# Kernel tuning notes

Hardware: AMD Instinct MI355X
Metric: run time of the kernel (lower is better)

Reference implementation:

```python
import jax, jax.numpy as jnp
import numpy as np

PAD = float(-2**32 + 1)


def setup_inputs() -> dict:
    key = jax.random.key(0)
    ks = jax.random.split(key, 10)
    B, S, D = 8, 1024, 1024
    s = 0.02  # keep projections in sane range
    return {
        "Q": jax.random.normal(ks[0], (B, S, D), jnp.float32),
        "K": jax.random.normal(ks[1], (B, S, D), jnp.float32),
        "V": jax.random.normal(ks[2], (B, S, D), jnp.float32),
        "WQ": jax.random.normal(ks[3], (D, D), jnp.float32) * s,
        "bQ": jnp.zeros((D,), jnp.float32),
        "WK": jax.random.normal(ks[4], (D, D), jnp.float32) * s,
        "bK": jnp.zeros((D,), jnp.float32),
        "WV": jax.random.normal(ks[5], (D, D), jnp.float32) * s,
        "bV": jnp.zeros((D,), jnp.float32),
        "WO": jax.random.normal(ks[6], (D, D), jnp.float32) * s,
        "bO": jnp.zeros((D,), jnp.float32),
        "h": 16,
    }


def reference(Q, K, V, WQ, bQ, WK, bK, WV, bV, WO, bO, h):
    B, S, D = Q.shape
    dk = D // h
    # Dense projections with relu activation (as in the Keras layer)
    Qp = jax.nn.relu(Q @ WQ + bQ)
    Kp = jax.nn.relu(K @ WK + bK)
    Vp = jax.nn.relu(V @ WV + bV)
    # tf.concat(tf.split(x, h, axis=2), axis=0): head-major stacking -> (h, B, S, dk)
    qh = Qp.reshape(B, S, h, dk).transpose(2, 0, 1, 3)
    kh = Kp.reshape(B, S, h, dk).transpose(2, 0, 1, 3)
    vh = Vp.reshape(B, S, h, dk).transpose(2, 0, 1, 3)
    # scaled dot product; NOTE: source scales by 1/sqrt(d_model), not 1/sqrt(d_k)
    scores = jnp.einsum('hbqd,hbkd->hbqk', qh, kh) / jnp.sqrt(jnp.float32(D))
    # key padding mask: zero key rows -> large negative
    kmask = jnp.sum(jnp.abs(kh), axis=-1) != 0  # (h,B,Tk)
    scores = jnp.where(kmask[:, :, None, :], scores, PAD)
    w = jax.nn.softmax(scores, axis=-1)
    # query padding mask: zero query rows -> zero weights
    qmask = jnp.sign(jnp.sum(jnp.abs(qh), axis=-1))  # (h,B,Tq), 0/1
    w = w * qmask[:, :, :, None]
    # dropout_prob = 0.0 -> identity
    out = jnp.einsum('hbqk,hbkd->hbqd', w, vh)
    # tf.concat(tf.split(dot_product, h, axis=0), axis=2) -> (B,S,h*dk)
    out = out.transpose(1, 2, 0, 3).reshape(B, S, D)
    return jax.nn.relu(out @ WO + bO)
```

## Files before the change

### kernel.cpp

```cpp
#include <hip/hip_runtime.h>
#include <hip/hip_bf16.h>
#include <cstdint>

#define DEV __device__ __forceinline__

typedef __attribute__((ext_vector_type(4))) float f32x4;
typedef __attribute__((ext_vector_type(8))) short b16x8;
typedef __attribute__((ext_vector_type(4))) unsigned short u16x4;
typedef __attribute__((ext_vector_type(8))) unsigned short u16x8;
typedef __attribute__((ext_vector_type(2))) unsigned int u32x2;

typedef __attribute__((address_space(1))) void gvoid_t;
typedef __attribute__((address_space(3))) void lvoid_t;

static constexpr int Bsz = 8, Ssz = 1024, Dsz = 1024;
static constexpr int Mrows = Bsz * Ssz;

DEV void gld16(const void* g, void* l) {
  __builtin_amdgcn_global_load_lds((gvoid_t*)(uintptr_t)g,
                                   (lvoid_t*)(unsigned)(uintptr_t)l, 16, 0, 0);
}

DEV unsigned short f2bf(float x) {
  unsigned int u = __float_as_uint(x);
  u += 0x7fffu + ((u >> 16) & 1u);
  return (unsigned short)(u >> 16);
}

DEV unsigned int cvt2(float lo, float hi) {
  __hip_bfloat162 h = __float22bfloat162_rn(make_float2(lo, hi));
  unsigned int u;
  __builtin_memcpy(&u, &h, 4);
  return u;
}

__global__ __launch_bounds__(256) void wconv_kernel(
    const float* __restrict__ WQ, const float* __restrict__ WK,
    const float* __restrict__ WV, const float* __restrict__ WO,
    unsigned short* __restrict__ Wt) {
  __shared__ float tile[64][65];
  const int w = blockIdx.z;
  const float* W = (w == 0) ? WQ : (w == 1) ? WK : (w == 2) ? WV : WO;
  const int k0 = blockIdx.x * 64, n0 = blockIdx.y * 64;
  const int t = threadIdx.x;
  {
    const int r = t >> 4;
    const int c = (t & 15) * 4;
#pragma unroll
    for (int i = 0; i < 4; ++i) {
      f32x4 v = *(const f32x4*)(W + (size_t)(k0 + i * 16 + r) * Dsz + n0 + c);
      tile[i * 16 + r][c + 0] = v[0];
      tile[i * 16 + r][c + 1] = v[1];
      tile[i * 16 + r][c + 2] = v[2];
      tile[i * 16 + r][c + 3] = v[3];
    }
  }
  __syncthreads();
  {
    const int n = t >> 2;
    const int ks = (t & 3) * 16;
    unsigned short* dst =
        Wt + (size_t)w * Dsz * Dsz + (size_t)(n0 + n) * Dsz + k0 + ks;
#pragma unroll
    for (int j = 0; j < 16; j += 4) {
      u16x4 p;
#pragma unroll
      for (int jj = 0; jj < 4; ++jj) p[jj] = f2bf(tile[ks + j + jj][n]);
      *(u16x4*)(dst + j) = p;
    }
  }
}

template <bool A_FP32, int OUT_MODE>
DEV void gemm_body(unsigned short* __restrict__ Asl,
                   unsigned short* __restrict__ Bsl,
                   const void* __restrict__ A_,
                   const unsigned short* __restrict__ Bt,
                   const float* __restrict__ bias, void* __restrict__ C_,
                   int m0, int n0, float outscale) {
  constexpr int Kd = 1024, Nd = 1024;
  const int t = threadIdx.x, lane = t & 63, wave = t >> 6;
  const int grp = lane >> 4, r16 = lane & 15;
  const int wm = wave >> 1, wn = wave & 1;
  const int swz = (r16 & 7) << 4;
  f32x4 acc[4][4] = {};
  for (int kt = 0; kt < Kd; kt += 64) {
#pragma unroll
    for (int j = 0; j < 4; ++j) {
      int chunk = (wave * 4 + j) * 64 + lane;
      int row = chunk >> 3, c = chunk & 7;
      int csw = c ^ (row & 7);
      gld16(Bt + (size_t)(n0 + row) * Kd + kt + csw * 8,
            (char*)Bsl + (wave * 4 + j) * 1024);
      if constexpr (!A_FP32) {
        gld16((const unsigned short*)A_ + (size_t)(m0 + row) * Kd + kt + csw * 8,
              (char*)Asl + (wave * 4 + j) * 1024);
      }
    }
    if constexpr (A_FP32) {
      const float* A = (const float*)A_;
#pragma unroll
      for (int it = 0; it < 4; ++it) {
        int chunk = it * 256 + t;
        int row = chunk >> 3, c = chunk & 7;
        int csw = c ^ (row & 7);
        const float* src = A + (size_t)(m0 + row) * Kd + kt + csw * 8;
        f32x4 v0 = *(const f32x4*)src;
        f32x4 v1 = *(const f32x4*)(src + 4);
        u32x2 w0, w1;
        w0[0] = cvt2(v0[0], v0[1]);
        w0[1] = cvt2(v0[2], v0[3]);
        w1[0] = cvt2(v1[0], v1[1]);
        w1[1] = cvt2(v1[2], v1[3]);
        *(u32x2*)((char*)Asl + chunk * 16) = w0;
        *(u32x2*)((char*)Asl + chunk * 16 + 8) = w1;
      }
    }
    __syncthreads();
#pragma unroll
    for (int cs = 0; cs < 2; ++cs) {
      b16x8 af[4], bfr[4];
#pragma unroll
      for (int mi = 0; mi < 4; ++mi)
        af[mi] = *(const b16x8*)((char*)Asl + (wm * 64 + mi * 16 + r16) * 128 +
                                 ((cs * 64 + grp * 16) ^ swz));
#pragma unroll
      for (int ni = 0; ni < 4; ++ni)
        bfr[ni] = *(const b16x8*)((char*)Bsl + (wn * 64 + ni * 16 + r16) * 128 +
                                  ((cs * 64 + grp * 16) ^ swz));
#pragma unroll
      for (int mi = 0; mi < 4; ++mi)
#pragma unroll
        for (int ni = 0; ni < 4; ++ni)
          acc[mi][ni] = __builtin_amdgcn_mfma_f32_16x16x32_bf16(
              af[mi], bfr[ni], acc[mi][ni], 0, 0, 0);
    }
    __syncthreads();
  }
#pragma unroll
  for (int mi = 0; mi < 4; ++mi) {
#pragma unroll
    for (int ni = 0; ni < 4; ++ni) {
      int col = n0 + wn * 64 + ni * 16 + r16;
      float bv = bias[col];
      int row0 = m0 + wm * 64 + mi * 16 + grp * 4;
      if constexpr (OUT_MODE == 2) {
        int bb = row0 >> 10, s = row0 & 1023;
        u16x4 pk;
#pragma unroll
        for (int r = 0; r < 4; ++r)
          pk[r] = f2bf(fmaxf(acc[mi][ni][r] + bv, 0.0f) * outscale);
        *(u16x4*)((unsigned short*)C_ +
                  (((size_t)(bb * 1024 + col)) << 10) + s) = pk;
      } else {
#pragma unroll
        for (int r = 0; r < 4; ++r) {
          float v = fmaxf(acc[mi][ni][r] + bv, 0.0f) * outscale;
          if constexpr (OUT_MODE == 1)
            ((unsigned short*)C_)[(size_t)(row0 + r) * Nd + col] = f2bf(v);
          else
            ((float*)C_)[(size_t)(row0 + r) * Nd + col] = v;
        }
      }
    }
  }
}

static constexpr float QSCALE = 0.03125f * 1.4426950408889634f;

__global__ __launch_bounds__(256) void proj3_kernel(
    const float* __restrict__ Q, const float* __restrict__ K,
    const float* __restrict__ V, const unsigned short* __restrict__ Wt,
    const float* __restrict__ bQ, const float* __restrict__ bK,
    const float* __restrict__ bV, unsigned short* __restrict__ Qp,
    unsigned short* __restrict__ Kp, unsigned short* __restrict__ VpT) {
  __shared__ unsigned short Asl[128 * 64] __attribute__((aligned(16)));
  __shared__ unsigned short Bsl[128 * 64] __attribute__((aligned(16)));
  const size_t DD = (size_t)Dsz * Dsz;
  const int bid = blockIdx.x;
  const int id2 = (bid & 7) * 64 + (bid >> 3);
  const int n0 = (id2 & 7) * 128, m0 = (id2 >> 3) * 128;
  const int z = blockIdx.z;
  if (z == 0)
    gemm_body<true, 1>(Asl, Bsl, Q, Wt, bQ, Qp, m0, n0, QSCALE);
  else if (z == 1)
    gemm_body<true, 1>(Asl, Bsl, K, Wt + DD, bK, Kp, m0, n0, 1.0f);
  else
    gemm_body<true, 2>(Asl, Bsl, V, Wt + 2 * DD, bV, VpT, m0, n0, 1.0f);
}

__global__ __launch_bounds__(256) void out_gemm_kernel(
    const unsigned short* __restrict__ AO,
    const unsigned short* __restrict__ WOt, const float* __restrict__ bO,
    float* __restrict__ Out) {
  __shared__ unsigned short Asl[128 * 64] __attribute__((aligned(16)));
  __shared__ unsigned short Bsl[128 * 64] __attribute__((aligned(16)));
  const int bid = blockIdx.x;
  const int id2 = (bid & 7) * 64 + (bid >> 3);
  const int n0 = (id2 & 7) * 128, m0 = (id2 >> 3) * 128;
  gemm_body<false, 0>(Asl, Bsl, AO, WOt, bO, Out, m0, n0, 1.0f);
}

__global__ __launch_bounds__(512, 4) void attn_kernel(
    const unsigned short* __restrict__ Qp, const unsigned short* __restrict__ Kp,
    const unsigned short* __restrict__ VpT, unsigned short* __restrict__ AO) {
  __shared__ unsigned short Ks[2][64 * 64] __attribute__((aligned(16)));
  __shared__ unsigned short Vs[2][64 * 64] __attribute__((aligned(16)));
  __shared__ unsigned short Ps[16][16 * 64] __attribute__((aligned(16)));
  const int t = threadIdx.x, lane = t & 63, wave = t >> 6;
  const int grp = lane >> 4, r16 = lane & 15;
  const int bid = blockIdx.x;
  const int id2 = (bid & 7) * 64 + (bid >> 3);
  const int q0 = (id2 & 3) * 256;
  const int bh = id2 >> 2;
  const int b = bh & 7, head = bh >> 3;

  const int srow = t >> 3, scc = t & 7;
  const int csw = scc ^ (srow & 7);
  const unsigned short* kbase = Kp + ((size_t)b * Ssz) * Dsz + head * 64;
  const unsigned short* vbase = VpT + ((size_t)b * Dsz + head * 64) * Ssz;

  const int sqA = q0 + wave * 16 + r16;
  const unsigned short* qbA = Qp + ((size_t)b * Ssz + sqA) * Dsz + head * 64;
  const unsigned short* qbB = qbA + (size_t)128 * Dsz;
  b16x8 qfA0 = *(const b16x8*)(qbA + grp * 8);
  b16x8 qfA1 = *(const b16x8*)(qbA + 32 + grp * 8);
  b16x8 qfB0 = *(const b16x8*)(qbB + grp * 8);
  b16x8 qfB1 = *(const b16x8*)(qbB + 32 + grp * 8);

  f32x4 oA[4] = {}, oB[4] = {};
  f32x4 olA = {}, olB = {};
  const f32x4 zero4 = {0.0f, 0.0f, 0.0f, 0.0f};
  const b16x8 ones = {16256, 16256, 16256, 16256,
                      16256, 16256, 16256, 16256};

  auto stage = [&](int kv0, int pb) {
    gld16(kbase + (size_t)(kv0 + srow) * Dsz + csw * 8,
          (char*)Ks[pb] + wave * 1024);
    gld16(vbase + (size_t)srow * Ssz + kv0 + csw * 8,
          (char*)Vs[pb] + wave * 1024);
  };

  stage(0, 0);
  __syncthreads();
  int cur = 0;

  for (int it = 0; it < 16; ++it) {
    if (it < 15) stage((it + 1) * 64, cur ^ 1);

    __builtin_amdgcn_s_setprio(1);
    f32x4 scA[4], scB[4];
#pragma unroll
    for (int f = 0; f < 4; ++f) {
      int k = f * 16 + r16;
      int kswz = (k & 7) << 4;
      const char* kb = (const char*)Ks[cur] + k * 128;
      b16x8 kf0 = *(const b16x8*)(kb + ((grp * 16) ^ kswz));
      b16x8 kf1 = *(const b16x8*)(kb + ((64 + grp * 16) ^ kswz));
      f32x4 sA = __builtin_amdgcn_mfma_f32_16x16x32_bf16(kf0, qfA0, zero4, 0, 0, 0);
      scA[f] = __builtin_amdgcn_mfma_f32_16x16x32_bf16(kf1, qfA1, sA, 0, 0, 0);
      f32x4 sB = __builtin_amdgcn_mfma_f32_16x16x32_bf16(kf0, qfB0, zero4, 0, 0, 0);
      scB[f] = __builtin_amdgcn_mfma_f32_16x16x32_bf16(kf1, qfB1, sB, 0, 0, 0);
    }
    __builtin_amdgcn_s_setprio(0);

    {
      int qs = (r16 & 7) << 4;
      char* prowA = (char*)Ps + (wave * 2 + 0) * 2048 + r16 * 128;
      char* prowB = (char*)Ps + (wave * 2 + 1) * 2048 + r16 * 128;
#pragma unroll
      for (int f = 0; f < 4; ++f) {
        u32x2 w;
        w[0] = cvt2(exp2f(scA[f][0]), exp2f(scA[f][1]));
        w[1] = cvt2(exp2f(scA[f][2]), exp2f(scA[f][3]));
        *(u32x2*)(prowA + ((f * 32 + grp * 8) ^ qs)) = w;
      }
#pragma unroll
      for (int f = 0; f < 4; ++f) {
        u32x2 w;
        w[0] = cvt2(exp2f(scB[f][0]), exp2f(scB[f][1]));
        w[1] = cvt2(exp2f(scB[f][2]), exp2f(scB[f][3]));
        *(u32x2*)(prowB + ((f * 32 + grp * 8) ^ qs)) = w;
      }
    }

    __builtin_amdgcn_s_setprio(1);
#pragma unroll
    for (int ks = 0; ks < 2; ++ks) {
      int pswz = (r16 & 7) << 4;
      int poff = r16 * 128 + ((ks * 64 + grp * 16) ^ pswz);
      b16x8 paA = *(const b16x8*)((char*)Ps + (wave * 2 + 0) * 2048 + poff);
      b16x8 paB = *(const b16x8*)((char*)Ps + (wave * 2 + 1) * 2048 + poff);
      olA = __builtin_amdgcn_mfma_f32_16x16x32_bf16(paA, ones, olA, 0, 0, 0);
      olB = __builtin_amdgcn_mfma_f32_16x16x32_bf16(paB, ones, olB, 0, 0, 0);
#pragma unroll
      for (int fc = 0; fc < 4; ++fc) {
        int d = fc * 16 + r16;
        int vswz = (d & 7) << 4;
        b16x8 vb = *(const b16x8*)((char*)Vs[cur] + d * 128 +
                                   ((ks * 64 + grp * 16) ^ vswz));
        oA[fc] = __builtin_amdgcn_mfma_f32_16x16x32_bf16(paA, vb, oA[fc], 0, 0, 0);
        oB[fc] = __builtin_amdgcn_mfma_f32_16x16x32_bf16(paB, vb, oB[fc], 0, 0, 0);
      }
    }
    __builtin_amdgcn_s_setprio(0);
    __syncthreads();
    cur ^= 1;
  }

#pragma unroll
  for (int fc = 0; fc < 4; ++fc) {
    int col = head * 64 + fc * 16 + r16;
#pragma unroll
    for (int r = 0; r < 4; ++r) {
      int rowA = q0 + wave * 16 + grp * 4 + r;
      AO[((size_t)b * Ssz + rowA) * Dsz + col] = f2bf(oA[fc][r] / olA[r]);
      AO[((size_t)b * Ssz + rowA + 128) * Dsz + col] = f2bf(oB[fc][r] / olB[r]);
    }
  }
}

extern "C" void kernel_launch(void* const* d_in, const int* in_sizes, int n_in,
                              void* d_out, int out_size, void* d_ws,
                              size_t ws_size, hipStream_t stream) {
  const float* Q = (const float*)d_in[0];
  const float* K = (const float*)d_in[1];
  const float* V = (const float*)d_in[2];
  const float* WQ = (const float*)d_in[3];
  const float* bQ = (const float*)d_in[4];
  const float* WK = (const float*)d_in[5];
  const float* bK = (const float*)d_in[6];
  const float* WV = (const float*)d_in[7];
  const float* bV = (const float*)d_in[8];
  const float* WO = (const float*)d_in[9];
  const float* bO = (const float*)d_in[10];

  char* ws = (char*)d_ws;
  const size_t MB = 1024ull * 1024ull;
  const size_t DD = (size_t)Dsz * Dsz;
  unsigned short* Wt = (unsigned short*)(ws);
  unsigned short* Qp = (unsigned short*)(ws + 8 * MB);
  unsigned short* Kp = (unsigned short*)(ws + 24 * MB);
  unsigned short* VpT = (unsigned short*)(ws + 40 * MB);
  unsigned short* AO = (unsigned short*)(ws + 56 * MB);

  wconv_kernel<<<dim3(16, 16, 4), 256, 0, stream>>>(WQ, WK, WV, WO, Wt);
  proj3_kernel<<<dim3(512, 1, 3), 256, 0, stream>>>(Q, K, V, Wt, bQ, bK, bV,
                                                    Qp, Kp, VpT);
  attn_kernel<<<512, 512, 0, stream>>>(Qp, Kp, VpT, AO);
  out_gemm_kernel<<<512, 256, 0, stream>>>(AO, Wt + 3 * DD, bO, (float*)d_out);
}
```

Measured before the change: 174.4 us.

## Software-pipeline fp32 A loads and double-buffer B in projection GEMM

Measured after the change: 168.8 us. -3.3%, faster.

```diff
diff --git a/kernel.cpp b/kernel.cpp
--- a/kernel.cpp
+++ b/kernel.cpp
@@ -9,6 +9,7 @@
 typedef __attribute__((ext_vector_type(4))) unsigned short u16x4;
 typedef __attribute__((ext_vector_type(8))) unsigned short u16x8;
 typedef __attribute__((ext_vector_type(2))) unsigned int u32x2;
+typedef __attribute__((ext_vector_type(4))) unsigned int u32x4;
 
 typedef __attribute__((address_space(1))) void gvoid_t;
 typedef __attribute__((address_space(3))) void lvoid_t;
@@ -71,13 +72,119 @@
   }
 }
 
-template <bool A_FP32, int OUT_MODE>
-DEV void gemm_body(unsigned short* __restrict__ Asl,
-                   unsigned short* __restrict__ Bsl,
-                   const void* __restrict__ A_,
-                   const unsigned short* __restrict__ Bt,
-                   const float* __restrict__ bias, void* __restrict__ C_,
-                   int m0, int n0, float outscale) {
+template <int OUT_MODE>
+DEV void gemm_body_f32(unsigned short* __restrict__ Asl,
+                       unsigned short* __restrict__ Bsl,
+                       const float* __restrict__ A,
+                       const unsigned short* __restrict__ Bt,
+                       const float* __restrict__ bias, void* __restrict__ C_,
+                       int m0, int n0, float outscale) {
+  constexpr int Kd = 1024, Nd = 1024;
+  const int t = threadIdx.x, lane = t & 63, wave = t >> 6;
+  const int grp = lane >> 4, r16 = lane & 15;
+  const int wm = wave >> 1, wn = wave & 1;
+  const int swz = (r16 & 7) << 4;
+  f32x4 acc[4][4] = {};
+  f32x4 areg[4][2];
+
+  auto loadA = [&](int kt) {
+#pragma unroll
+    for (int it = 0; it < 4; ++it) {
+      int chunk = it * 256 + t;
+      int row = chunk >> 3, c = chunk & 7;
+      int csw = c ^ (row & 7);
+      const float* src = A + (size_t)(m0 + row) * Kd + kt + csw * 8;
+      areg[it][0] = *(const f32x4*)src;
+      areg[it][1] = *(const f32x4*)(src + 4);
+    }
+  };
+  auto writeA = [&]() {
+#pragma unroll
+    for (int it = 0; it < 4; ++it) {
+      int chunk = it * 256 + t;
+      u32x4 w;
+      w[0] = cvt2(areg[it][0][0], areg[it][0][1]);
+      w[1] = cvt2(areg[it][0][2], areg[it][0][3]);
+      w[2] = cvt2(areg[it][1][0], areg[it][1][1]);
+      w[3] = cvt2(areg[it][1][2], areg[it][1][3]);
+      *(u32x4*)((char*)Asl + chunk * 16) = w;
+    }
+  };
+  auto stageB = [&](int kt, int pb) {
+#pragma unroll
+    for (int j = 0; j < 4; ++j) {
+      int chunk = (wave * 4 + j) * 64 + lane;
+      int row = chunk >> 3, c = chunk & 7;
+      int csw = c ^ (row & 7);
+      gld16(Bt + (size_t)(n0 + row) * Kd + kt + csw * 8,
+            (char*)Bsl + pb * 16384 + (wave * 4 + j) * 1024);
+    }
+  };
+
+  loadA(0);
+  stageB(0, 0);
+  int cur = 0;
+  for (int kt = 0; kt < Kd; kt += 64) {
+    writeA();
+    __syncthreads();
+    if (kt < Kd - 64) {
+      stageB(kt + 64, cur ^ 1);
+      loadA(kt + 64);
+    }
+#pragma unroll
+    for (int cs = 0; cs < 2; ++cs) {
+      b16x8 af[4], bfr[4];
+#pragma unroll
+      for (int mi = 0; mi < 4; ++mi)
+        af[mi] = *(const b16x8*)((char*)Asl + (wm * 64 + mi * 16 + r16) * 128 +
+                                 ((cs * 64 + grp * 16) ^ swz));
+#pragma unroll
+      for (int ni = 0; ni < 4; ++ni)
+        bfr[ni] = *(const b16x8*)((char*)Bsl + cur * 16384 +
+                                  (wn * 64 + ni * 16 + r16) * 128 +
+                                  ((cs * 64 + grp * 16) ^ swz));
+#pragma unroll
+      for (int mi = 0; mi < 4; ++mi)
+#pragma unroll
+        for (int ni = 0; ni < 4; ++ni)
+          acc[mi][ni] = __builtin_amdgcn_mfma_f32_16x16x32_bf16(
+              af[mi], bfr[ni], acc[mi][ni], 0, 0, 0);
+    }
+    __syncthreads();
+    cur ^= 1;
+  }
+#pragma unroll
+  for (int mi = 0; mi < 4; ++mi) {
+#pragma unroll
+    for (int ni = 0; ni < 4; ++ni) {
+      int col = n0 + wn * 64 + ni * 16 + r16;
+      float bv = bias[col];
+      int row0 = m0 + wm * 64 + mi * 16 + grp * 4;
+      if constexpr (OUT_MODE == 2) {
+        int bb = row0 >> 10, s = row0 & 1023;
+        u16x4 pk;
+#pragma unroll
+        for (int r = 0; r < 4; ++r)
+          pk[r] = f2bf(fmaxf(acc[mi][ni][r] + bv, 0.0f) * outscale);
+        *(u16x4*)((unsigned short*)C_ +
+                  (((size_t)(bb * 1024 + col)) << 10) + s) = pk;
+      } else {
+#pragma unroll
+        for (int r = 0; r < 4; ++r) {
+          float v = fmaxf(acc[mi][ni][r] + bv, 0.0f) * outscale;
+          ((unsigned short*)C_)[(size_t)(row0 + r) * Nd + col] = f2bf(v);
+        }
+      }
+    }
+  }
+}
+
+DEV void gemm_body_bf16(unsigned short* __restrict__ Asl,
+                        unsigned short* __restrict__ Bsl,
+                        const unsigned short* __restrict__ A,
+                        const unsigned short* __restrict__ Bt,
+                        const float* __restrict__ bias, float* __restrict__ C_,
+                        int m0, int n0) {
   constexpr int Kd = 1024, Nd = 1024;
   const int t = threadIdx.x, lane = t & 63, wave = t >> 6;
   const int grp = lane >> 4, r16 = lane & 15;
@@ -92,29 +199,8 @@
       int csw = c ^ (row & 7);
       gld16(Bt + (size_t)(n0 + row) * Kd + kt + csw * 8,
             (char*)Bsl + (wave * 4 + j) * 1024);
-      if constexpr (!A_FP32) {
-        gld16((const unsigned short*)A_ + (size_t)(m0 + row) * Kd + kt + csw * 8,
-              (char*)Asl + (wave * 4 + j) * 1024);
-      }
-    }
-    if constexpr (A_FP32) {
-      const float* A = (const float*)A_;
-#pragma unroll
-      for (int it = 0; it < 4; ++it) {
-        int chunk = it * 256 + t;
-        int row = chunk >> 3, c = chunk & 7;
-        int csw = c ^ (row & 7);
-        const float* src = A + (size_t)(m0 + row) * Kd + kt + csw * 8;
-        f32x4 v0 = *(const f32x4*)src;
-        f32x4 v1 = *(const f32x4*)(src + 4);
-        u32x2 w0, w1;
-        w0[0] = cvt2(v0[0], v0[1]);
-        w0[1] = cvt2(v0[2], v0[3]);
-        w1[0] = cvt2(v1[0], v1[1]);
-        w1[1] = cvt2(v1[2], v1[3]);
-        *(u32x2*)((char*)Asl + chunk * 16) = w0;
-        *(u32x2*)((char*)Asl + chunk * 16 + 8) = w1;
-      }
+      gld16(A + (size_t)(m0 + row) * Kd + kt + csw * 8,
+            (char*)Asl + (wave * 4 + j) * 1024);
     }
     __syncthreads();
 #pragma unroll
@@ -144,23 +230,10 @@
       int col = n0 + wn * 64 + ni * 16 + r16;
       float bv = bias[col];
       int row0 = m0 + wm * 64 + mi * 16 + grp * 4;
-      if constexpr (OUT_MODE == 2) {
-        int bb = row0 >> 10, s = row0 & 1023;
-        u16x4 pk;
-#pragma unroll
-        for (int r = 0; r < 4; ++r)
-          pk[r] = f2bf(fmaxf(acc[mi][ni][r] + bv, 0.0f) * outscale);
-        *(u16x4*)((unsigned short*)C_ +
-                  (((size_t)(bb * 1024 + col)) << 10) + s) = pk;
-      } else {
-#pragma unroll
-        for (int r = 0; r < 4; ++r) {
-          float v = fmaxf(acc[mi][ni][r] + bv, 0.0f) * outscale;
-          if constexpr (OUT_MODE == 1)
-            ((unsigned short*)C_)[(size_t)(row0 + r) * Nd + col] = f2bf(v);
-          else
-            ((float*)C_)[(size_t)(row0 + r) * Nd + col] = v;
-        }
+#pragma unroll
+      for (int r = 0; r < 4; ++r) {
+        float v = fmaxf(acc[mi][ni][r] + bv, 0.0f);
+        C_[(size_t)(row0 + r) * Nd + col] = v;
       }
     }
   }
@@ -175,18 +248,18 @@
     const float* __restrict__ bV, unsigned short* __restrict__ Qp,
     unsigned short* __restrict__ Kp, unsigned short* __restrict__ VpT) {
   __shared__ unsigned short Asl[128 * 64] __attribute__((aligned(16)));
-  __shared__ unsigned short Bsl[128 * 64] __attribute__((aligned(16)));
+  __shared__ unsigned short Bsl[2 * 128 * 64] __attribute__((aligned(16)));
   const size_t DD = (size_t)Dsz * Dsz;
   const int bid = blockIdx.x;
   const int id2 = (bid & 7) * 64 + (bid >> 3);
   const int n0 = (id2 & 7) * 128, m0 = (id2 >> 3) * 128;
   const int z = blockIdx.z;
   if (z == 0)
-    gemm_body<true, 1>(Asl, Bsl, Q, Wt, bQ, Qp, m0, n0, QSCALE);
+    gemm_body_f32<1>(Asl, Bsl, Q, Wt, bQ, Qp, m0, n0, QSCALE);
   else if (z == 1)
-    gemm_body<true, 1>(Asl, Bsl, K, Wt + DD, bK, Kp, m0, n0, 1.0f);
+    gemm_body_f32<1>(Asl, Bsl, K, Wt + DD, bK, Kp, m0, n0, 1.0f);
   else
-    gemm_body<true, 2>(Asl, Bsl, V, Wt + 2 * DD, bV, VpT, m0, n0, 1.0f);
+    gemm_body_f32<2>(Asl, Bsl, V, Wt + 2 * DD, bV, VpT, m0, n0, 1.0f);
 }
 
 __global__ __launch_bounds__(256) void out_gemm_kernel(
@@ -198,7 +271,7 @@
   const int bid = blockIdx.x;
   const int id2 = (bid & 7) * 64 + (bid >> 3);
   const int n0 = (id2 & 7) * 128, m0 = (id2 >> 3) * 128;
-  gemm_body<false, 0>(Asl, Bsl, AO, WOt, bO, Out, m0, n0, 1.0f);
+  gemm_body_bf16(Asl, Bsl, AO, WOt, bO, Out, m0, n0);
 }
 
 __global__ __launch_bounds__(512, 4) void attn_kernel(
```
